# Optimization experiments

Hardware: AMD Instinct MI355X
Metric: run time of the kernel (lower is better)

## Reference

```python
import jax, jax.numpy as jnp
import numpy as np

D_MODEL = 256
B = 4
Q_PER_IMAGE = 256
FEATS_PER_IMAGE = 65536
HW = 512


def setup_inputs() -> dict:
    key = jax.random.key(0)
    ks = jax.random.split(key, 12)
    queries = jax.random.normal(ks[0], (B * Q_PER_IMAGE, D_MODEL), dtype=jnp.float32)
    feature_values = jax.random.normal(ks[1], (B * FEATS_PER_IMAGE, D_MODEL), dtype=jnp.float32)
    # sparse COO indices of the full-scale feature map: (batch, h, w), batch-sorted
    batch_col = jnp.repeat(jnp.arange(B, dtype=jnp.int64), FEATS_PER_IMAGE)
    hw = jax.random.randint(ks[2], (B * FEATS_PER_IMAGE, 2), 0, HW).astype(jnp.int64)
    feature_indices = jnp.concatenate([batch_col[:, None], hw], axis=-1)
    query_batch_offsets = (jnp.arange(B, dtype=jnp.int64) * Q_PER_IMAGE)
    # MLP params: torch nn.Linear convention y = x @ W.T + b, W: [out, in]
    scale = 1.0 / np.sqrt(D_MODEL)
    params = {}
    for i in range(4):
        params[f"W{i+1}"] = jax.random.uniform(ks[3 + 2 * i], (D_MODEL, D_MODEL), jnp.float32, -scale, scale)
        params[f"b{i+1}"] = jax.random.uniform(ks[4 + 2 * i], (D_MODEL,), jnp.float32, -scale, scale)
    return {
        "queries": queries,
        "feature_values": feature_values,
        "feature_indices": feature_indices,
        "query_batch_offsets": query_batch_offsets,
        **params,
    }


def reference(queries, feature_values, feature_indices, query_batch_offsets,
              W1, b1, W2, b2, W3, b3, W4, b4):
    x = queries
    for W, b in ((W1, b1), (W2, b2), (W3, b3)):
        x = jax.nn.relu(x @ W.T + b)
    x = x @ W4.T + b4  # [B*Q, d]

    nb = query_batch_offsets.shape[0]
    d = x.shape[-1]
    q = x.reshape(nb, -1, d)                    # [B, Q, d] per-image query splits
    feats = feature_values.reshape(nb, -1, d)   # [B, Nf, d] per-image feature splits
    # per-image torch.mm(im_feats, im_queries.T), batched
    logits = jnp.einsum("bnd,bqd->bnq", feats, q)  # values of the output sparse COO tensor
    # Output sparse indices are (feature_indices[i], q) for each local query q;
    # the values (in index order) are exactly `logits`.
    return logits
```

## Files before the change

### kernel.cpp

```cpp
#include <hip/hip_runtime.h>
#include <hip/hip_bf16.h>

#define D_MODEL 256
#define N_ROWS  262144
#define N_Q     1024
#define ROWS_PER_BATCH 65536

typedef __attribute__((ext_vector_type(8))) short short8;
typedef __attribute__((ext_vector_type(16))) float floatx16;

static __device__ __forceinline__ short f2bf(float x) {
    union { __hip_bfloat16 h; short s; } u;
    u.h = __float2bfloat16(x);
    return u.s;
}

__global__ __launch_bounds__(256) void mlp_kernel(
    const float* __restrict__ q,
    const float* __restrict__ W1, const float* __restrict__ b1,
    const float* __restrict__ W2, const float* __restrict__ b2,
    const float* __restrict__ W3, const float* __restrict__ b3,
    const float* __restrict__ W4, const float* __restrict__ b4,
    __hip_bfloat16* __restrict__ xout)
{
    __shared__ float cur[4][D_MODEL];
    const int j = threadIdx.x;
    const int row0 = blockIdx.x * 4;

    #pragma unroll
    for (int i = 0; i < 4; i++)
        cur[i][j] = q[(long)(row0 + i) * D_MODEL + j];
    __syncthreads();

    const float* Ws[4] = { W1, W2, W3, W4 };
    const float* bs[4] = { b1, b2, b3, b4 };

    for (int l = 0; l < 4; l++) {
        const float4* wrow = (const float4*)(Ws[l] + (long)j * D_MODEL);
        float acc0 = bs[l][j];
        float acc1 = acc0, acc2 = acc0, acc3 = acc0;
        #pragma unroll 8
        for (int k = 0; k < D_MODEL / 4; k++) {
            float4 w  = wrow[k];
            float4 c0 = ((const float4*)cur[0])[k];
            float4 c1 = ((const float4*)cur[1])[k];
            float4 c2 = ((const float4*)cur[2])[k];
            float4 c3 = ((const float4*)cur[3])[k];
            acc0 += w.x*c0.x + w.y*c0.y + w.z*c0.z + w.w*c0.w;
            acc1 += w.x*c1.x + w.y*c1.y + w.z*c1.z + w.w*c1.w;
            acc2 += w.x*c2.x + w.y*c2.y + w.z*c2.z + w.w*c2.w;
            acc3 += w.x*c3.x + w.y*c3.y + w.z*c3.z + w.w*c3.w;
        }
        __syncthreads();
        if (l < 3) {
            cur[0][j] = fmaxf(acc0, 0.f);
            cur[1][j] = fmaxf(acc1, 0.f);
            cur[2][j] = fmaxf(acc2, 0.f);
            cur[3][j] = fmaxf(acc3, 0.f);
            __syncthreads();
        } else {
            xout[(long)(row0 + 0) * D_MODEL + j] = __float2bfloat16(acc0);
            xout[(long)(row0 + 1) * D_MODEL + j] = __float2bfloat16(acc1);
            xout[(long)(row0 + 2) * D_MODEL + j] = __float2bfloat16(acc2);
            xout[(long)(row0 + 3) * D_MODEL + j] = __float2bfloat16(acc3);
        }
    }
}

__global__ __launch_bounds__(256) void logits_kernel(
    const float* __restrict__ F,
    const __hip_bfloat16* __restrict__ X,
    float* __restrict__ out)
{
    const int wave = threadIdx.x >> 6;
    const int lane = threadIdx.x & 63;
    const int m    = lane & 31;
    const int kg   = lane >> 5;

    const long row0  = (long)blockIdx.x * 64;
    const int  batch = (int)(row0 >> 16);

    const float* a0 = F + (row0 + m) * D_MODEL + kg * 8;
    const float* a1 = a0 + 32 * D_MODEL;

    const __hip_bfloat16* bb = X + ((long)(batch << 8) + (wave << 6) + m) * D_MODEL + kg * 8;
    const __hip_bfloat16* b0 = bb;
    const __hip_bfloat16* b1 = bb + 32 * D_MODEL;

    floatx16 acc00 = {0.f}, acc01 = {0.f}, acc10 = {0.f}, acc11 = {0.f};

    #pragma unroll 2
    for (int ks = 0; ks < 16; ks++) {
        const int k0 = ks * 16;

        float4 a0lo = *(const float4*)(a0 + k0);
        float4 a0hi = *(const float4*)(a0 + k0 + 4);
        float4 a1lo = *(const float4*)(a1 + k0);
        float4 a1hi = *(const float4*)(a1 + k0 + 4);

        short8 bf0 = *(const short8*)(b0 + k0);
        short8 bf1 = *(const short8*)(b1 + k0);

        short8 af0 = { f2bf(a0lo.x), f2bf(a0lo.y), f2bf(a0lo.z), f2bf(a0lo.w),
                       f2bf(a0hi.x), f2bf(a0hi.y), f2bf(a0hi.z), f2bf(a0hi.w) };
        short8 af1 = { f2bf(a1lo.x), f2bf(a1lo.y), f2bf(a1lo.z), f2bf(a1lo.w),
                       f2bf(a1hi.x), f2bf(a1hi.y), f2bf(a1hi.z), f2bf(a1hi.w) };

        acc00 = __builtin_amdgcn_mfma_f32_32x32x16_bf16(af0, bf0, acc00, 0, 0, 0);
        acc01 = __builtin_amdgcn_mfma_f32_32x32x16_bf16(af0, bf1, acc01, 0, 0, 0);
        acc10 = __builtin_amdgcn_mfma_f32_32x32x16_bf16(af1, bf0, acc10, 0, 0, 0);
        acc11 = __builtin_amdgcn_mfma_f32_32x32x16_bf16(af1, bf1, acc11, 0, 0, 0);
    }

    const int colbase = (wave << 6) + m;
    #pragma unroll
    for (int rt = 0; rt < 2; rt++) {
        const floatx16 accr0 = (rt == 0) ? acc00 : acc10;
        const floatx16 accr1 = (rt == 0) ? acc01 : acc11;
        const long rbase = row0 + rt * 32 + 4 * kg;
        #pragma unroll
        for (int reg = 0; reg < 16; reg++) {
            const int r = (reg & 3) + 8 * (reg >> 2);
            out[(rbase + r) * D_MODEL + colbase]      = accr0[reg];
            out[(rbase + r) * D_MODEL + colbase + 32] = accr1[reg];
        }
    }
}

extern "C" void kernel_launch(void* const* d_in, const int* in_sizes, int n_in,
                              void* d_out, int out_size, void* d_ws, size_t ws_size,
                              hipStream_t stream) {
    const float* queries = (const float*)d_in[0];
    const float* feats   = (const float*)d_in[1];
    const float* W1 = (const float*)d_in[4];
    const float* b1 = (const float*)d_in[5];
    const float* W2 = (const float*)d_in[6];
    const float* b2 = (const float*)d_in[7];
    const float* W3 = (const float*)d_in[8];
    const float* b3 = (const float*)d_in[9];
    const float* W4 = (const float*)d_in[10];
    const float* b4 = (const float*)d_in[11];

    __hip_bfloat16* x_bf16 = (__hip_bfloat16*)d_ws;

    mlp_kernel<<<N_Q / 4, 256, 0, stream>>>(queries, W1, b1, W2, b2, W3, b3, W4, b4, x_bf16);
    logits_kernel<<<N_ROWS / 64, 256, 0, stream>>>(feats, x_bf16, (float*)d_out);
}
```

Before: 648.2 us.

## Stage feature tile in LDS as bf16 shared across all four waves

In the old code each of the four waves loaded the same 64x256 fp32 feature tile from global memory and converted it to bf16 separately. Now the block loads the tile once with coalesced float4 reads, converts it to bf16 and stores it in padded shared memory. The MFMA loop then reads the A fragments from LDS. This cuts redundant global or cache traffic and repeated conversion work by four times, at the cost of about 33KB of LDS per block (lower occupancy) and a barrier before compute. The unroll factor also rises from 2 to 4.

```diff
diff --git a/kernel.cpp b/kernel.cpp
--- a/kernel.cpp
+++ b/kernel.cpp
@@ -4,7 +4,6 @@
 #define D_MODEL 256
 #define N_ROWS  262144
 #define N_Q     1024
-#define ROWS_PER_BATCH 65536
 
 typedef __attribute__((ext_vector_type(8))) short short8;
 typedef __attribute__((ext_vector_type(16))) float floatx16;
@@ -67,44 +66,54 @@
     }
 }
 
+#define APAD 264
+
 __global__ __launch_bounds__(256) void logits_kernel(
     const float* __restrict__ F,
     const __hip_bfloat16* __restrict__ X,
     float* __restrict__ out)
 {
-    const int wave = threadIdx.x >> 6;
-    const int lane = threadIdx.x & 63;
+    __shared__ __hip_bfloat16 As[64 * APAD];
+
+    const int t    = threadIdx.x;
+    const int wave = t >> 6;
+    const int lane = t & 63;
     const int m    = lane & 31;
     const int kg   = lane >> 5;
 
     const long row0  = (long)blockIdx.x * 64;
     const int  batch = (int)(row0 >> 16);
 
-    const float* a0 = F + (row0 + m) * D_MODEL + kg * 8;
-    const float* a1 = a0 + 32 * D_MODEL;
+    const float* Fbase = F + row0 * D_MODEL;
+    #pragma unroll
+    for (int i = 0; i < 16; i++) {
+        const int flat = i * 256 + t;
+        const int row  = flat >> 6;
+        const int c4   = (flat & 63) << 2;
+        float4 v = *(const float4*)(Fbase + (size_t)flat * 4);
+        union { ushort4 u; short s[4]; } w;
+        w.s[0] = f2bf(v.x); w.s[1] = f2bf(v.y);
+        w.s[2] = f2bf(v.z); w.s[3] = f2bf(v.w);
+        *(ushort4*)(&As[row * APAD + c4]) = w.u;
+    }
+    __syncthreads();
 
+    const __hip_bfloat16* a0 = &As[m * APAD + kg * 8];
+    const __hip_bfloat16* a1 = a0 + 32 * APAD;
     const __hip_bfloat16* bb = X + ((long)(batch << 8) + (wave << 6) + m) * D_MODEL + kg * 8;
     const __hip_bfloat16* b0 = bb;
     const __hip_bfloat16* b1 = bb + 32 * D_MODEL;
 
     floatx16 acc00 = {0.f}, acc01 = {0.f}, acc10 = {0.f}, acc11 = {0.f};
 
-    #pragma unroll 2
+    #pragma unroll 4
     for (int ks = 0; ks < 16; ks++) {
         const int k0 = ks * 16;
 
-        float4 a0lo = *(const float4*)(a0 + k0);
-        float4 a0hi = *(const float4*)(a0 + k0 + 4);
-        float4 a1lo = *(const float4*)(a1 + k0);
-        float4 a1hi = *(const float4*)(a1 + k0 + 4);
-
+        short8 af0 = *(const short8*)(a0 + k0);
+        short8 af1 = *(const short8*)(a1 + k0);
         short8 bf0 = *(const short8*)(b0 + k0);
         short8 bf1 = *(const short8*)(b1 + k0);
-
-        short8 af0 = { f2bf(a0lo.x), f2bf(a0lo.y), f2bf(a0lo.z), f2bf(a0lo.w),
-                       f2bf(a0hi.x), f2bf(a0hi.y), f2bf(a0hi.z), f2bf(a0hi.w) };
-        short8 af1 = { f2bf(a1lo.x), f2bf(a1lo.y), f2bf(a1lo.z), f2bf(a1lo.w),
-                       f2bf(a1hi.x), f2bf(a1hi.y), f2bf(a1hi.z), f2bf(a1hi.w) };
 
         acc00 = __builtin_amdgcn_mfma_f32_32x32x16_bf16(af0, bf0, acc00, 0, 0, 0);
         acc01 = __builtin_amdgcn_mfma_f32_32x32x16_bf16(af0, bf1, acc01, 0, 0, 0);
```

Result: faster. 553.0 us (-14.7%).
